# Kernel optimization log

Hardware: AMD Instinct MI355X
Metric: run time of the kernel (lower is better)

Reference implementation:

```python
import jax, jax.numpy as jnp
from jax import lax
import numpy as np

ALPHA = 0.5   # weight of shape vs temporal component
GAMMA = 0.01  # soft-min temperature
BIG = 1e10    # finite stand-in for +inf borders (safe gradients)


def _softmin3(a, b, c, gamma):
    # -gamma * logsumexp(-x/gamma) over the three candidates
    z = jnp.stack([a, b, c], axis=0)
    return -gamma * jax.nn.logsumexp(-z / gamma, axis=0)


def _softdtw(D, gamma):
    """Soft-DTW value per problem. D: (B, N, N) cost matrix -> (B,).
    Classic DP: R[i,j] = D[i-1,j-1] + softmin(R[i-1,j-1], R[i-1,j], R[i,j-1])."""
    B, N, _ = D.shape
    # R row 0: R[0,0]=0, R[0,j>=1]=inf
    row0 = jnp.concatenate(
        [jnp.zeros((B, 1), D.dtype), jnp.full((B, N), BIG, D.dtype)], axis=1)
    left_init = jnp.full((B,), BIG, D.dtype)  # R[i,0] = inf for i>=1

    def row_step(R_prev, d_row):  # d_row: (B, N) = D[:, i-1, :]
        # per column j: diag = R_prev[j-1], up = R_prev[j], left = carry
        xs = (d_row.T, R_prev[:, :-1].T, R_prev[:, 1:].T)  # each (N, B)

        def col_step(r_left, x):
            d, r_diag, r_up = x
            r = d + _softmin3(r_diag, r_up, r_left, gamma)
            return r, r

        _, vals = lax.scan(col_step, left_init, xs)  # (N, B)
        R_row = jnp.concatenate([left_init[:, None], vals.T], axis=1)  # (B, N+1)
        return R_row, None

    R_last, _ = lax.scan(row_step, row0, jnp.transpose(D, (1, 0, 2)))
    return R_last[:, -1]  # R[N, N]


def _dilate(inp, tgt):
    B, C, N = inp.shape
    t = tgt.reshape(B * C, N)
    p = inp.reshape(B * C, N)
    # pairwise squared distances between 1-d points: D[k,i,j] = (t_i - p_j)^2
    D = (t[:, :, None] - p[:, None, :]) ** 2  # (B*C, N, N)

    # shape loss = soft-DTW value, averaged over channels
    sdtw = _softdtw(D, GAMMA)  # (B*C,)
    loss_shape = sdtw.reshape(B, C).mean(axis=1)  # (B,)

    # soft alignment path = gradient of soft-DTW w.r.t. the cost matrix
    E = jax.grad(lambda d: _softdtw(d, GAMMA).sum())(D)  # (B*C, N, N)

    # Omega[i,j] = (i - j)^2 temporal penalty
    idx = jnp.arange(1, N + 1, dtype=D.dtype)
    Omega = (idx[:, None] - idx[None, :]) ** 2  # (N, N)

    lt = jnp.sum(E * Omega, axis=(1, 2)) / (N * N)  # (B*C,)
    loss_temporal = lt.reshape(B, C).mean(axis=1)  # (B,)

    loss = (ALPHA * loss_shape + (1.0 - ALPHA) * loss_temporal).mean()
    return loss, loss_shape, loss_temporal


def setup_inputs() -> dict:
    key = jax.random.key(0)
    k1, k2 = jax.random.split(key)
    B, C, N = 64, 8, 160
    return {
        "input": jax.random.normal(k1, (B, C, N), jnp.float32),
        "target": jax.random.normal(k2, (B, C, N), jnp.float32),
    }


def reference(input, target):
    return _dilate(input, target)
```

## Files before the change

kernel.cpp:

```cpp
#include <hip/hip_runtime.h>
#include <math.h>


#define NN     160
#define BC_TOT 512
#define B_SZ   64
#define C_SZ   8
#define BIGC2  1e12f
#define SC2    12.01122405f
#define GLN2   0.0069314718056f
#define KPH    16
#define NCHUNK 20
#define NPHASE 22
#define RSZ    328

__device__ __forceinline__ float fexp2(float x) {
#if __has_builtin(__builtin_amdgcn_exp2f)
    return __builtin_amdgcn_exp2f(x);
#else
    return exp2f(x);
#endif
}
__device__ __forceinline__ float flog2(float x) {
#if __has_builtin(__builtin_amdgcn_logf)
    return __builtin_amdgcn_logf(x);
#else
    return log2f(x);
#endif
}
__device__ __forceinline__ float frcp(float x) {
#if __has_builtin(__builtin_amdgcn_rcpf)
    return __builtin_amdgcn_rcpf(x);
#else
    return 1.0f / x;
#endif
}
__device__ __forceinline__ float dpp_up1_inj(float old, float x) {
    int oi = __builtin_bit_cast(int, old);
    int xi = __builtin_bit_cast(int, x);
    return __builtin_bit_cast(float,
        __builtin_amdgcn_update_dpp(oi, xi, 0x138, 0xF, 0xF, false));
}
__device__ __forceinline__ void barrier_lds() {
    __asm__ __volatile__("" ::: "memory");
    __builtin_amdgcn_s_waitcnt(0xC07F);
    __builtin_amdgcn_s_barrier();
    __asm__ __volatile__("" ::: "memory");
}

__global__ __launch_bounds__(192)
void dtw_fwd_kernel(const float* __restrict__ input,
                    const float* __restrict__ target,
                    float* __restrict__ sdtw,
                    float* __restrict__ wlt)
{
    const int k    = blockIdx.x;
    const int tid  = threadIdx.x;
    const int w    = tid >> 6;
    const int lane = tid & 63;
    const bool rowok = (tid < NN);

    __shared__ __align__(16) float  Pp[4][520];
    __shared__ __align__(16) float2 bRG[2][RSZ];

    const float* tg = target + (size_t)k * NN;
    const float* pg = input  + (size_t)k * NN;
    for (int x = tid; x < 520; x += 192) {
        #pragma unroll
        for (int s = 0; s < 4; ++s) {
            const int v = x + s - 192;
            Pp[s][x] = ((unsigned)v < (unsigned)NN) ? pg[v] * SC2 : 0.0f;
        }
    }
    for (int x = tid; x < 2 * RSZ; x += 192) {
        float2 z; z.x = BIGC2; z.y = 0.0f;
        ((float2*)bRG)[x] = z;
    }
    const float trS = rowok ? tg[tid] * SC2 : 0.0f;
    barrier_lds();

    const bool isL0    = (lane == 0);
    const bool isL63p  = (lane == 63) && (w < 2);
    const bool useRing = (w > 0);
    const int  ti2     = 2 * (tid + 1);

    const int cLoF = 4 * w;
    const int cHiF = (4 * w + 13 < NCHUNK - 1) ? 4 * w + 13 : NCHUNK - 1;

    float r1c2 = BIGC2, u1c2 = BIGC2, u2c2 = BIGC2;
    float s1 = 0.0f, v1 = 0.0f, v2 = 0.0f;

    for (int t = 0; t < NPHASE; ++t) {
        const int c = t - w;
        if (c >= cLoF && c <= cHiF) {
            const int dlo = 2 + c * KPH;
            float rgx[18], rgd[18];
            if (useRing) {
                const float4* q = (const float4*)&bRG[w - 1][dlo - 2];
                #pragma unroll
                for (int x = 0; x < 9; ++x) {
                    const float4 v4 = q[x];
                    rgx[2 * x]     = v4.x; rgd[2 * x]     = v4.y;
                    rgx[2 * x + 1] = v4.z; rgd[2 * x + 1] = v4.w;
                }
            } else {
                #pragma unroll
                for (int x = 0; x < 18; ++x) { rgx[x] = BIGC2; rgd[x] = 0.0f; }
                if (c == 0) rgx[0] = 0.0f;
            }
            float pvvS[KPH];
            {
                const int A  = 192 - tid + KPH * c;
                const int sA = A & 3;
                const float4* pq = (const float4*)&Pp[sA][A - sA];
                #pragma unroll
                for (int x = 0; x < 4; ++x) {
                    const float4 p4 = pq[x];
                    pvvS[4 * x]     = p4.x; pvvS[4 * x + 1] = p4.y;
                    pvvS[4 * x + 2] = p4.z; pvvS[4 * x + 3] = p4.w;
                }
            }
            if (c == cLoF) {
                u1c2 = isL0 ? rgx[1] : BIGC2;
                u2c2 = isL0 ? rgx[0] : BIGC2;
                v1   = isL0 ? rgd[1] : 0.0f;
                v2   = isL0 ? rgd[0] : 0.0f;
            }
            float djf = (float)(dlo - ti2);
            #pragma unroll
            for (int u = 0; u < KPH; ++u) {
                const int d = dlo + u;
                const float vdC = u2c2;
                const float vuC = u1c2;
                const float vlC = r1c2;
                const float gd = v2, gu = v1, gl = s1;
                const float mnC = fminf(vdC, fminf(vuC, vlC));
                const float ed = fexp2(mnC - vdC);
                const float ev = fexp2(mnC - vuC);
                const float eh = fexp2(mnC - vlC);
                const float ss = ed + ev + eh;
                const float rs = frcp(ss);
                const float dtS = trS - pvvS[u];
                const float rC2 = __builtin_fmaf(dtS, dtS, mnC) - flog2(ss);
                const float num = __builtin_fmaf(ed, gd,
                                  __builtin_fmaf(ev, gu, eh * gl));
                const float rdot = __builtin_fmaf(num, rs, djf * djf);
                if (isL63p) {
                    float2 pub; pub.x = rC2; pub.y = rdot;
                    bRG[w][d] = pub;
                }
                if (d == 2 * NN) {
                    if (tid == NN - 1) {
                        sdtw[k] = rC2 * GLN2;
                        wlt[k]  = rdot * (1.0f / (NN * NN));
                    }
                }
                u2c2 = u1c2;
                u1c2 = dpp_up1_inj(rgx[u + 2], rC2);
                v2 = v1;
                v1 = dpp_up1_inj(rgd[u + 2], rdot);
                r1c2 = rC2;
                s1   = rdot;
                djf += 1.0f;
            }
        }
        barrier_lds();
    }
}

__global__ __launch_bounds__(64)
void finalize_kernel(const float* __restrict__ sdtw,
                     const float* __restrict__ wlt,
                     float* __restrict__ out)
{
    const int b = threadIdx.x;
    float ls = 0.0f, lt = 0.0f;
    #pragma unroll
    for (int c = 0; c < C_SZ; ++c) {
        ls += sdtw[b * C_SZ + c];
        lt += wlt[b * C_SZ + c];
    }
    ls *= (1.0f / C_SZ);
    lt *= (1.0f / C_SZ);
    out[1 + b]        = ls;
    out[1 + B_SZ + b] = lt;
    float v = 0.5f * ls + 0.5f * lt;
    #pragma unroll
    for (int o = 32; o > 0; o >>= 1) v += __shfl_down(v, o);
    if (b == 0) out[0] = v * (1.0f / B_SZ);
}

extern "C" void kernel_launch(void* const* d_in, const int* in_sizes, int n_in,
                              void* d_out, int out_size, void* d_ws, size_t ws_size,
                              hipStream_t stream) {
    const float* input  = (const float*)d_in[0];
    const float* target = (const float*)d_in[1];
    float* out = (float*)d_out;

    float* sdtw = (float*)d_ws;
    float* wlt  = sdtw + BC_TOT;

    dtw_fwd_kernel<<<BC_TOT, 192, 0, stream>>>(input, target, sdtw, wlt);
    finalize_kernel<<<1, 64, 0, stream>>>(sdtw, wlt, out);
}
```

Baseline: 93.69 us.

## Process two DTW problems per block to interleave independent recurrences

Each block now computes two independent soft-DTW problems at once, interleaving their wavefront recurrences in the same instruction stream and halving the grid to 256 blocks. The idea is instruction-level parallelism: the serial dependency chain of exp/log/rcp per cell can be hidden by the second problem's independent work, and the per-phase barrier and ring-exchange overhead is amortised over two problems. The cost is doubled register pressure (two sets of ring and pvv arrays), wider LDS traffic, and fewer blocks, leaving 256 workgroups on a GPU with 256 CUs.

```diff
diff --git a/kernel.cpp b/kernel.cpp
--- a/kernel.cpp
+++ b/kernel.cpp
@@ -54,29 +54,34 @@
                     float* __restrict__ sdtw,
                     float* __restrict__ wlt)
 {
-    const int k    = blockIdx.x;
+    const int kA   = 2 * blockIdx.x;
     const int tid  = threadIdx.x;
     const int w    = tid >> 6;
     const int lane = tid & 63;
     const bool rowok = (tid < NN);
 
-    __shared__ __align__(16) float  Pp[4][520];
-    __shared__ __align__(16) float2 bRG[2][RSZ];
-
-    const float* tg = target + (size_t)k * NN;
-    const float* pg = input  + (size_t)k * NN;
+    __shared__ __align__(16) float  Pp[2][4][520];
+    __shared__ __align__(16) float4 bRG[2][RSZ];
+
+    const float* tgA = target + (size_t)kA * NN;
+    const float* pgA = input  + (size_t)kA * NN;
+    const float* tgB = tgA + NN;
+    const float* pgB = pgA + NN;
     for (int x = tid; x < 520; x += 192) {
         #pragma unroll
         for (int s = 0; s < 4; ++s) {
             const int v = x + s - 192;
-            Pp[s][x] = ((unsigned)v < (unsigned)NN) ? pg[v] * SC2 : 0.0f;
+            const bool ok = ((unsigned)v < (unsigned)NN);
+            Pp[0][s][x] = ok ? pgA[v] * SC2 : 0.0f;
+            Pp[1][s][x] = ok ? pgB[v] * SC2 : 0.0f;
         }
     }
     for (int x = tid; x < 2 * RSZ; x += 192) {
-        float2 z; z.x = BIGC2; z.y = 0.0f;
-        ((float2*)bRG)[x] = z;
-    }
-    const float trS = rowok ? tg[tid] * SC2 : 0.0f;
+        float4 z; z.x = BIGC2; z.y = 0.0f; z.z = BIGC2; z.w = 0.0f;
+        ((float4*)bRG)[x] = z;
+    }
+    const float trA = rowok ? tgA[tid] * SC2 : 0.0f;
+    const float trB = rowok ? tgB[tid] * SC2 : 0.0f;
     barrier_lds();
 
     const bool isL0    = (lane == 0);
@@ -87,80 +92,101 @@
     const int cLoF = 4 * w;
     const int cHiF = (4 * w + 13 < NCHUNK - 1) ? 4 * w + 13 : NCHUNK - 1;
 
-    float r1c2 = BIGC2, u1c2 = BIGC2, u2c2 = BIGC2;
-    float s1 = 0.0f, v1 = 0.0f, v2 = 0.0f;
+    float r1A = BIGC2, u1A = BIGC2, u2A = BIGC2;
+    float s1A = 0.0f,  v1A = 0.0f,  v2A = 0.0f;
+    float r1B = BIGC2, u1B = BIGC2, u2B = BIGC2;
+    float s1B = 0.0f,  v1B = 0.0f,  v2B = 0.0f;
 
     for (int t = 0; t < NPHASE; ++t) {
         const int c = t - w;
         if (c >= cLoF && c <= cHiF) {
             const int dlo = 2 + c * KPH;
-            float rgx[18], rgd[18];
+            float rgxA[18], rgdA[18], rgxB[18], rgdB[18];
             if (useRing) {
-                const float4* q = (const float4*)&bRG[w - 1][dlo - 2];
+                const float4* q = &bRG[w - 1][dlo - 2];
                 #pragma unroll
-                for (int x = 0; x < 9; ++x) {
+                for (int x = 0; x < 18; ++x) {
                     const float4 v4 = q[x];
-                    rgx[2 * x]     = v4.x; rgd[2 * x]     = v4.y;
-                    rgx[2 * x + 1] = v4.z; rgd[2 * x + 1] = v4.w;
+                    rgxA[x] = v4.x; rgdA[x] = v4.y;
+                    rgxB[x] = v4.z; rgdB[x] = v4.w;
                 }
             } else {
                 #pragma unroll
-                for (int x = 0; x < 18; ++x) { rgx[x] = BIGC2; rgd[x] = 0.0f; }
-                if (c == 0) rgx[0] = 0.0f;
-            }
-            float pvvS[KPH];
+                for (int x = 0; x < 18; ++x) {
+                    rgxA[x] = BIGC2; rgdA[x] = 0.0f;
+                    rgxB[x] = BIGC2; rgdB[x] = 0.0f;
+                }
+                if (c == 0) { rgxA[0] = 0.0f; rgxB[0] = 0.0f; }
+            }
+            float pvvA[KPH], pvvB[KPH];
             {
                 const int A  = 192 - tid + KPH * c;
                 const int sA = A & 3;
-                const float4* pq = (const float4*)&Pp[sA][A - sA];
+                const float4* qa = (const float4*)&Pp[0][sA][A - sA];
+                const float4* qb = (const float4*)&Pp[1][sA][A - sA];
                 #pragma unroll
                 for (int x = 0; x < 4; ++x) {
-                    const float4 p4 = pq[x];
-                    pvvS[4 * x]     = p4.x; pvvS[4 * x + 1] = p4.y;
-                    pvvS[4 * x + 2] = p4.z; pvvS[4 * x + 3] = p4.w;
+                    const float4 a4 = qa[x];
+                    const float4 b4 = qb[x];
+                    pvvA[4 * x]     = a4.x; pvvA[4 * x + 1] = a4.y;
+                    pvvA[4 * x + 2] = a4.z; pvvA[4 * x + 3] = a4.w;
+                    pvvB[4 * x]     = b4.x; pvvB[4 * x + 1] = b4.y;
+                    pvvB[4 * x + 2] = b4.z; pvvB[4 * x + 3] = b4.w;
                 }
             }
             if (c == cLoF) {
-                u1c2 = isL0 ? rgx[1] : BIGC2;
-                u2c2 = isL0 ? rgx[0] : BIGC2;
-                v1   = isL0 ? rgd[1] : 0.0f;
-                v2   = isL0 ? rgd[0] : 0.0f;
+                u1A = isL0 ? rgxA[1] : BIGC2;  u2A = isL0 ? rgxA[0] : BIGC2;
+                v1A = isL0 ? rgdA[1] : 0.0f;   v2A = isL0 ? rgdA[0] : 0.0f;
+                u1B = isL0 ? rgxB[1] : BIGC2;  u2B = isL0 ? rgxB[0] : BIGC2;
+                v1B = isL0 ? rgdB[1] : 0.0f;   v2B = isL0 ? rgdB[0] : 0.0f;
             }
             float djf = (float)(dlo - ti2);
             #pragma unroll
             for (int u = 0; u < KPH; ++u) {
                 const int d = dlo + u;
-                const float vdC = u2c2;
-                const float vuC = u1c2;
-                const float vlC = r1c2;
-                const float gd = v2, gu = v1, gl = s1;
-                const float mnC = fminf(vdC, fminf(vuC, vlC));
-                const float ed = fexp2(mnC - vdC);
-                const float ev = fexp2(mnC - vuC);
-                const float eh = fexp2(mnC - vlC);
-                const float ss = ed + ev + eh;
-                const float rs = frcp(ss);
-                const float dtS = trS - pvvS[u];
-                const float rC2 = __builtin_fmaf(dtS, dtS, mnC) - flog2(ss);
-                const float num = __builtin_fmaf(ed, gd,
-                                  __builtin_fmaf(ev, gu, eh * gl));
-                const float rdot = __builtin_fmaf(num, rs, djf * djf);
+                const float om = djf * djf;
+                const float mnA = fminf(u2A, fminf(u1A, r1A));
+                const float edA = fexp2(mnA - u2A);
+                const float evA = fexp2(mnA - u1A);
+                const float ehA = fexp2(mnA - r1A);
+                const float ssA = edA + evA + ehA;
+                const float rsA = frcp(ssA);
+                const float dtA = trA - pvvA[u];
+                const float rCA = __builtin_fmaf(dtA, dtA, mnA) - flog2(ssA);
+                const float numA = __builtin_fmaf(edA, v2A,
+                                   __builtin_fmaf(evA, v1A, ehA * s1A));
+                const float rdA = __builtin_fmaf(numA, rsA, om);
+                const float mnB = fminf(u2B, fminf(u1B, r1B));
+                const float edB = fexp2(mnB - u2B);
+                const float evB = fexp2(mnB - u1B);
+                const float ehB = fexp2(mnB - r1B);
+                const float ssB = edB + evB + ehB;
+                const float rsB = frcp(ssB);
+                const float dtB = trB - pvvB[u];
+                const float rCB = __builtin_fmaf(dtB, dtB, mnB) - flog2(ssB);
+                const float numB = __builtin_fmaf(edB, v2B,
+                                   __builtin_fmaf(evB, v1B, ehB * s1B));
+                const float rdB = __builtin_fmaf(numB, rsB, om);
+
                 if (isL63p) {
-                    float2 pub; pub.x = rC2; pub.y = rdot;
+                    float4 pub;
+                    pub.x = rCA; pub.y = rdA; pub.z = rCB; pub.w = rdB;
                     bRG[w][d] = pub;
                 }
                 if (d == 2 * NN) {
                     if (tid == NN - 1) {
-                        sdtw[k] = rC2 * GLN2;
-                        wlt[k]  = rdot * (1.0f / (NN * NN));
+                        sdtw[kA]     = rCA * GLN2;
+                        wlt[kA]      = rdA * (1.0f / (NN * NN));
+                        sdtw[kA + 1] = rCB * GLN2;
+                        wlt[kA + 1]  = rdB * (1.0f / (NN * NN));
                     }
                 }
-                u2c2 = u1c2;
-                u1c2 = dpp_up1_inj(rgx[u + 2], rC2);
-                v2 = v1;
-                v1 = dpp_up1_inj(rgd[u + 2], rdot);
-                r1c2 = rC2;
-                s1   = rdot;
+                u2A = u1A; u1A = dpp_up1_inj(rgxA[u + 2], rCA);
+                v2A = v1A; v1A = dpp_up1_inj(rgdA[u + 2], rdA);
+                r1A = rCA; s1A = rdA;
+                u2B = u1B; u1B = dpp_up1_inj(rgxB[u + 2], rCB);
+                v2B = v1B; v1B = dpp_up1_inj(rgdB[u + 2], rdB);
+                r1B = rCB; s1B = rdB;
                 djf += 1.0f;
             }
         }
@@ -200,6 +226,6 @@
     float* sdtw = (float*)d_ws;
     float* wlt  = sdtw + BC_TOT;
 
-    dtw_fwd_kernel<<<BC_TOT, 192, 0, stream>>>(input, target, sdtw, wlt);
+    dtw_fwd_kernel<<<BC_TOT / 2, 192, 0, stream>>>(input, target, sdtw, wlt);
     finalize_kernel<<<1, 64, 0, stream>>>(sdtw, wlt, out);
 }
```

After: 105.6 us. 12.7% more time.

## Process all row bands in one wavefront sequentially, dropping inter-wave barriers

Applied to the files above, without the earlier changes.

Each block now runs a single 64-lane wavefront that works through the three 64-row bands one after another, instead of three wavefronts pipelined across phases with a block barrier after every phase. The boundary ring buffer shrinks to one shared row, overwritten in place. The next chunk's LDS window is double-buffered into registers before the current chunk is computed. This removes barrier and idle-wave cost but makes each block's serial dependency chain longer, since the bands no longer overlap in time.

```diff
diff --git a/kernel.cpp b/kernel.cpp
--- a/kernel.cpp
+++ b/kernel.cpp
@@ -10,8 +10,6 @@
 #define SC2    12.01122405f
 #define GLN2   0.0069314718056f
 #define KPH    16
-#define NCHUNK 20
-#define NPHASE 22
 #define RSZ    328
 
 __device__ __forceinline__ float fexp2(float x) {
@@ -48,123 +46,120 @@
     __asm__ __volatile__("" ::: "memory");
 }
 
-__global__ __launch_bounds__(192)
+#define LOAD_WIN(c_, rgx_, rgd_, pvv_) do {                                   \
+    const int dlo_ = 2 + (c_) * KPH;                                          \
+    if (w > 0) {                                                              \
+        const float4* q_ = (const float4*)&bRG[dlo_ - 2];                     \
+        _Pragma("unroll")                                                     \
+        for (int x_ = 0; x_ < 9; ++x_) {                                      \
+            const float4 v4_ = q_[x_];                                        \
+            rgx_[2 * x_]     = v4_.x; rgd_[2 * x_]     = v4_.y;               \
+            rgx_[2 * x_ + 1] = v4_.z; rgd_[2 * x_ + 1] = v4_.w;               \
+        }                                                                     \
+    } else {                                                                  \
+        _Pragma("unroll")                                                     \
+        for (int x_ = 0; x_ < 18; ++x_) { rgx_[x_] = BIGC2; rgd_[x_] = 0.0f; }\
+        if ((c_) == 0) rgx_[0] = 0.0f;           \
+    }                                                                         \
+    const int A_  = 192 - (64 * w + lane) + KPH * (c_);                       \
+    const int sA_ = A_ & 3;                                                   \
+    const float4* pq_ = (const float4*)&Pp[sA_][A_ - sA_];                    \
+    _Pragma("unroll")                                                         \
+    for (int x_ = 0; x_ < 4; ++x_) {                                          \
+        const float4 p4_ = pq_[x_];                                           \
+        pvv_[4 * x_]     = p4_.x; pvv_[4 * x_ + 1] = p4_.y;                   \
+        pvv_[4 * x_ + 2] = p4_.z; pvv_[4 * x_ + 3] = p4_.w;                   \
+    }                                                                         \
+} while (0)
+
+#define COMP_CHUNK(c_, rgx_, rgd_, pvv_) do {                                 \
+    const int dlo_ = 2 + (c_) * KPH;                                          \
+    if ((c_) == cLo) {         \
+        u1 = isL0 ? rgx_[1] : BIGC2;  u2 = isL0 ? rgx_[0] : BIGC2;            \
+        v1 = isL0 ? rgd_[1] : 0.0f;   v2 = isL0 ? rgd_[0] : 0.0f;             \
+    }                                                                         \
+    float djf_ = (float)(dlo_ - ti2);                       \
+    _Pragma("unroll")                                                         \
+    for (int u_ = 0; u_ < KPH; ++u_) {                                        \
+        const int d_ = dlo_ + u_;                                             \
+        const float mn = fminf(u2, fminf(u1, r1));                            \
+        const float ed = fexp2(mn - u2);         \
+        const float ev = fexp2(mn - u1);                                      \
+        const float eh = fexp2(mn - r1);                                      \
+        const float ss = ed + ev + eh;                              \
+        const float rs = frcp(ss);                                            \
+        const float dt = trS - pvv_[u_];                                      \
+        const float rC = __builtin_fmaf(dt, dt, mn) - flog2(ss);              \
+        const float nm = __builtin_fmaf(ed, v2,                               \
+                         __builtin_fmaf(ev, v1, eh * s1));                    \
+        const float rd = __builtin_fmaf(nm, rs, djf_ * djf_);                 \
+        if (pub) { float2 pb; pb.x = rC; pb.y = rd; bRG[d_] = pb; }           \
+        if (d_ == 2 * NN) {                                                   \
+            if (w == 2 && lane == NN - 1 - 128) {         \
+                sdtw[k] = rC * GLN2;                                          \
+                wlt[k]  = rd * (1.0f / (NN * NN));                            \
+            }                                                                 \
+        }                                                                     \
+        u2 = u1; u1 = dpp_up1_inj(rgx_[u_ + 2], rC);     \
+        v2 = v1; v1 = dpp_up1_inj(rgd_[u_ + 2], rd);                          \
+        r1 = rC; s1 = rd;                                                     \
+        djf_ += 1.0f;                                                         \
+    }                                                                         \
+} while (0)
+
+__global__ __launch_bounds__(64)
 void dtw_fwd_kernel(const float* __restrict__ input,
                     const float* __restrict__ target,
                     float* __restrict__ sdtw,
                     float* __restrict__ wlt)
 {
     const int k    = blockIdx.x;
-    const int tid  = threadIdx.x;
-    const int w    = tid >> 6;
-    const int lane = tid & 63;
-    const bool rowok = (tid < NN);
+    const int lane = threadIdx.x;
 
     __shared__ __align__(16) float  Pp[4][520];
-    __shared__ __align__(16) float2 bRG[2][RSZ];
+    __shared__ __align__(16) float2 bRG[RSZ];
 
     const float* tg = target + (size_t)k * NN;
     const float* pg = input  + (size_t)k * NN;
-    for (int x = tid; x < 520; x += 192) {
+    for (int x = lane; x < 520; x += 64) {
         #pragma unroll
         for (int s = 0; s < 4; ++s) {
             const int v = x + s - 192;
             Pp[s][x] = ((unsigned)v < (unsigned)NN) ? pg[v] * SC2 : 0.0f;
         }
     }
-    for (int x = tid; x < 2 * RSZ; x += 192) {
+    for (int x = lane; x < RSZ; x += 64) {
         float2 z; z.x = BIGC2; z.y = 0.0f;
-        ((float2*)bRG)[x] = z;
-    }
-    const float trS = rowok ? tg[tid] * SC2 : 0.0f;
+        bRG[x] = z;
+    }
+    const float tr0 = tg[lane] * SC2;
+    const float tr1 = tg[64 + lane] * SC2;
+    const float tr2 = (lane < NN - 128) ? tg[128 + lane] * SC2 : 0.0f;
     barrier_lds();
 
-    const bool isL0    = (lane == 0);
-    const bool isL63p  = (lane == 63) && (w < 2);
-    const bool useRing = (w > 0);
-    const int  ti2     = 2 * (tid + 1);
-
-    const int cLoF = 4 * w;
-    const int cHiF = (4 * w + 13 < NCHUNK - 1) ? 4 * w + 13 : NCHUNK - 1;
-
-    float r1c2 = BIGC2, u1c2 = BIGC2, u2c2 = BIGC2;
-    float s1 = 0.0f, v1 = 0.0f, v2 = 0.0f;
-
-    for (int t = 0; t < NPHASE; ++t) {
-        const int c = t - w;
-        if (c >= cLoF && c <= cHiF) {
-            const int dlo = 2 + c * KPH;
-            float rgx[18], rgd[18];
-            if (useRing) {
-                const float4* q = (const float4*)&bRG[w - 1][dlo - 2];
-                #pragma unroll
-                for (int x = 0; x < 9; ++x) {
-                    const float4 v4 = q[x];
-                    rgx[2 * x]     = v4.x; rgd[2 * x]     = v4.y;
-                    rgx[2 * x + 1] = v4.z; rgd[2 * x + 1] = v4.w;
-                }
-            } else {
-                #pragma unroll
-                for (int x = 0; x < 18; ++x) { rgx[x] = BIGC2; rgd[x] = 0.0f; }
-                if (c == 0) rgx[0] = 0.0f;
-            }
-            float pvvS[KPH];
-            {
-                const int A  = 192 - tid + KPH * c;
-                const int sA = A & 3;
-                const float4* pq = (const float4*)&Pp[sA][A - sA];
-                #pragma unroll
-                for (int x = 0; x < 4; ++x) {
-                    const float4 p4 = pq[x];
-                    pvvS[4 * x]     = p4.x; pvvS[4 * x + 1] = p4.y;
-                    pvvS[4 * x + 2] = p4.z; pvvS[4 * x + 3] = p4.w;
-                }
-            }
-            if (c == cLoF) {
-                u1c2 = isL0 ? rgx[1] : BIGC2;
-                u2c2 = isL0 ? rgx[0] : BIGC2;
-                v1   = isL0 ? rgd[1] : 0.0f;
-                v2   = isL0 ? rgd[0] : 0.0f;
-            }
-            float djf = (float)(dlo - ti2);
-            #pragma unroll
-            for (int u = 0; u < KPH; ++u) {
-                const int d = dlo + u;
-                const float vdC = u2c2;
-                const float vuC = u1c2;
-                const float vlC = r1c2;
-                const float gd = v2, gu = v1, gl = s1;
-                const float mnC = fminf(vdC, fminf(vuC, vlC));
-                const float ed = fexp2(mnC - vdC);
-                const float ev = fexp2(mnC - vuC);
-                const float eh = fexp2(mnC - vlC);
-                const float ss = ed + ev + eh;
-                const float rs = frcp(ss);
-                const float dtS = trS - pvvS[u];
-                const float rC2 = __builtin_fmaf(dtS, dtS, mnC) - flog2(ss);
-                const float num = __builtin_fmaf(ed, gd,
-                                  __builtin_fmaf(ev, gu, eh * gl));
-                const float rdot = __builtin_fmaf(num, rs, djf * djf);
-                if (isL63p) {
-                    float2 pub; pub.x = rC2; pub.y = rdot;
-                    bRG[w][d] = pub;
-                }
-                if (d == 2 * NN) {
-                    if (tid == NN - 1) {
-                        sdtw[k] = rC2 * GLN2;
-                        wlt[k]  = rdot * (1.0f / (NN * NN));
-                    }
-                }
-                u2c2 = u1c2;
-                u1c2 = dpp_up1_inj(rgx[u + 2], rC2);
-                v2 = v1;
-                v1 = dpp_up1_inj(rgd[u + 2], rdot);
-                r1c2 = rC2;
-                s1   = rdot;
-                djf += 1.0f;
-            }
+    const bool isL0 = (lane == 0);
+
+    for (int w = 0; w < 3; ++w) {
+        __asm__ __volatile__("" ::: "memory");
+        const int  cLo = 4 * w;
+        const int  cHi = (4 * w + 13 < 19) ? 4 * w + 13 : 19;
+        const bool pub = (lane == 63) && (w < 2);
+        const float trS = (w == 0) ? tr0 : (w == 1) ? tr1 : tr2;
+        const int  ti2 = 2 * (64 * w + lane + 1);
+
+        float r1 = BIGC2, u1 = BIGC2, u2 = BIGC2;
+        float s1 = 0.0f,  v1 = 0.0f,  v2 = 0.0f;
+
+        float rgxA[18], rgdA[18], pvvA[16];
+        float rgxB[18], rgdB[18], pvvB[16];
+
+        LOAD_WIN(cLo, rgxA, rgdA, pvvA);
+        for (int c = cLo; c <= cHi; c += 2) {
+            LOAD_WIN(c + 1, rgxB, rgdB, pvvB);
+            COMP_CHUNK(c, rgxA, rgdA, pvvA);
+            if (c + 2 <= cHi) LOAD_WIN(c + 2, rgxA, rgdA, pvvA);
+            COMP_CHUNK(c + 1, rgxB, rgdB, pvvB);
         }
-        barrier_lds();
     }
 }
 
@@ -200,6 +195,6 @@
     float* sdtw = (float*)d_ws;
     float* wlt  = sdtw + BC_TOT;
 
-    dtw_fwd_kernel<<<BC_TOT, 192, 0, stream>>>(input, target, sdtw, wlt);
+    dtw_fwd_kernel<<<BC_TOT, 64, 0, stream>>>(input, target, sdtw, wlt);
     finalize_kernel<<<1, 64, 0, stream>>>(sdtw, wlt, out);
 }
```

After: 110.7 us. +18.1%, slower.

## Replace block barriers with LDS flag spin-waits between wavefronts in soft-DTW wavefront

Applied to the files above, without the earlier changes.

Block-wide barriers per phase are replaced by per-wave progress flags in LDS. Each downstream wave spins on its upstream wave's counter before reading the boundary ring. The chunk size is halved to 8 anti-diagonals, so the pipeline fill skew between the three waves shrinks. The ring buffer is no longer initialized, and correctness relies on ordering of the publishing lane's LDS writes before the flag store. Spin-polling adds LDS traffic and the risk of subtle visibility issues.

```diff
diff --git a/kernel.cpp b/kernel.cpp
--- a/kernel.cpp
+++ b/kernel.cpp
@@ -9,10 +9,9 @@
 #define BIGC2  1e12f
 #define SC2    12.01122405f
 #define GLN2   0.0069314718056f
-#define KPH    16
-#define NCHUNK 20
-#define NPHASE 22
-#define RSZ    328
+#define KPH    8
+#define NCH    28
+#define RSZ    360
 
 __device__ __forceinline__ float fexp2(float x) {
 #if __has_builtin(__builtin_amdgcn_exp2f)
@@ -48,7 +47,7 @@
     __asm__ __volatile__("" ::: "memory");
 }
 
-__global__ __launch_bounds__(192)
+__global__ __launch_bounds__(192, 1)
 void dtw_fwd_kernel(const float* __restrict__ input,
                     const float* __restrict__ target,
                     float* __restrict__ sdtw,
@@ -58,10 +57,10 @@
     const int tid  = threadIdx.x;
     const int w    = tid >> 6;
     const int lane = tid & 63;
-    const bool rowok = (tid < NN);
 
     __shared__ __align__(16) float  Pp[4][520];
     __shared__ __align__(16) float2 bRG[2][RSZ];
+    __shared__ int flags[2];
 
     const float* tg = target + (size_t)k * NN;
     const float* pg = input  + (size_t)k * NN;
@@ -72,99 +71,105 @@
             Pp[s][x] = ((unsigned)v < (unsigned)NN) ? pg[v] * SC2 : 0.0f;
         }
     }
-    for (int x = tid; x < 2 * RSZ; x += 192) {
-        float2 z; z.x = BIGC2; z.y = 0.0f;
-        ((float2*)bRG)[x] = z;
-    }
-    const float trS = rowok ? tg[tid] * SC2 : 0.0f;
+    if (tid < 2) flags[tid] = 0;
+    const float trS = (tid < NN) ? tg[tid] * SC2 : 0.0f;
     barrier_lds();
 
     const bool isL0    = (lane == 0);
-    const bool isL63p  = (lane == 63) && (w < 2);
-    const bool useRing = (w > 0);
+    const bool pubw    = (w < 2);
+    const bool isL63p  = (lane == 63) && pubw;
     const int  ti2     = 2 * (tid + 1);
-
-    const int cLoF = 4 * w;
-    const int cHiF = (4 * w + 13 < NCHUNK - 1) ? 4 * w + 13 : NCHUNK - 1;
-
-    float r1c2 = BIGC2, u1c2 = BIGC2, u2c2 = BIGC2;
-    float s1 = 0.0f, v1 = 0.0f, v2 = 0.0f;
-
-    for (int t = 0; t < NPHASE; ++t) {
-        const int c = t - w;
-        if (c >= cLoF && c <= cHiF) {
-            const int dlo = 2 + c * KPH;
-            float rgx[18], rgd[18];
-            if (useRing) {
-                const float4* q = (const float4*)&bRG[w - 1][dlo - 2];
-                #pragma unroll
-                for (int x = 0; x < 9; ++x) {
-                    const float4 v4 = q[x];
-                    rgx[2 * x]     = v4.x; rgd[2 * x]     = v4.y;
-                    rgx[2 * x + 1] = v4.z; rgd[2 * x + 1] = v4.w;
+    const int  c0      = 8 * w;
+    const unsigned fPrevA = (unsigned)(unsigned long long)&flags[(w > 0) ? (w - 1) : 0];
+
+    float r1 = BIGC2, u1 = BIGC2, u2 = BIGC2;
+    float s1 = 0.0f,  v1 = 0.0f,  v2 = 0.0f;
+
+    for (int c = c0; c < c0 + NCH; ++c) {
+        if (w > 0) {
+            int fv;
+            for (;;) {
+                asm volatile("ds_read_b32 %0, %1\n\ts_waitcnt lgkmcnt(0)"
+                             : "=v"(fv) : "v"(fPrevA) : "memory");
+                if (__builtin_amdgcn_readfirstlane(fv) >= c + 1) break;
+            }
+        }
+        const int dlo = 2 + c * KPH;
+        float rgx[10], rgd[10];
+        if (w > 0) {
+            const float4* q = (const float4*)&bRG[w - 1][dlo - 2];
+            #pragma unroll
+            for (int x = 0; x < 5; ++x) {
+                const float4 v4 = q[x];
+                rgx[2 * x]     = v4.x; rgd[2 * x]     = v4.y;
+                rgx[2 * x + 1] = v4.z; rgd[2 * x + 1] = v4.w;
+            }
+        } else {
+            #pragma unroll
+            for (int x = 0; x < 10; ++x) { rgx[x] = BIGC2; rgd[x] = 0.0f; }
+            if (c == 0) rgx[0] = 0.0f;
+        }
+        float pvv[KPH];
+        {
+            const int A  = 192 - tid + KPH * c;
+            const int sA = A & 3;
+            const float4* pq = (const float4*)&Pp[sA][A - sA];
+            #pragma unroll
+            for (int x = 0; x < 2; ++x) {
+                const float4 p4 = pq[x];
+                pvv[4 * x]     = p4.x; pvv[4 * x + 1] = p4.y;
+                pvv[4 * x + 2] = p4.z; pvv[4 * x + 3] = p4.w;
+            }
+        }
+        if (c == c0) {
+            u1 = isL0 ? rgx[1] : BIGC2;  u2 = isL0 ? rgx[0] : BIGC2;
+            v1 = isL0 ? rgd[1] : 0.0f;   v2 = isL0 ? rgd[0] : 0.0f;
+        }
+        float djf = (float)(dlo - ti2);
+        #pragma unroll
+        for (int u = 0; u < KPH; ++u) {
+            const int d = dlo + u;
+            const float vdC = u2;
+            const float vuC = u1;
+            const float vlC = r1;
+            const float gd = v2, gu = v1, gl = s1;
+            const float mnC = fminf(vdC, fminf(vuC, vlC));
+            const float ed = fexp2(mnC - vdC);
+            const float ev = fexp2(mnC - vuC);
+            const float eh = fexp2(mnC - vlC);
+            const float ss = ed + ev + eh;
+            const float rs = frcp(ss);
+            const float dtS = trS - pvv[u];
+            const float rC2 = __builtin_fmaf(dtS, dtS, mnC) - flog2(ss);
+            const float num = __builtin_fmaf(ed, gd,
+                              __builtin_fmaf(ev, gu, eh * gl));
+            const float rdot = __builtin_fmaf(num, rs, djf * djf);
+            if (isL63p) {
+                float2 pb; pb.x = rC2; pb.y = rdot;
+                bRG[w][d] = pb;
+            }
+            if (d == 2 * NN) {
+                if (tid == NN - 1) {
+                    sdtw[k] = rC2 * GLN2;
+                    wlt[k]  = rdot * (1.0f / (NN * NN));
                 }
-            } else {
-                #pragma unroll
-                for (int x = 0; x < 18; ++x) { rgx[x] = BIGC2; rgd[x] = 0.0f; }
-                if (c == 0) rgx[0] = 0.0f;
-            }
-            float pvvS[KPH];
-            {
-                const int A  = 192 - tid + KPH * c;
-                const int sA = A & 3;
-                const float4* pq = (const float4*)&Pp[sA][A - sA];
-                #pragma unroll
-                for (int x = 0; x < 4; ++x) {
-                    const float4 p4 = pq[x];
-                    pvvS[4 * x]     = p4.x; pvvS[4 * x + 1] = p4.y;
-                    pvvS[4 * x + 2] = p4.z; pvvS[4 * x + 3] = p4.w;
-                }
-            }
-            if (c == cLoF) {
-                u1c2 = isL0 ? rgx[1] : BIGC2;
-                u2c2 = isL0 ? rgx[0] : BIGC2;
-                v1   = isL0 ? rgd[1] : 0.0f;
-                v2   = isL0 ? rgd[0] : 0.0f;
-            }
-            float djf = (float)(dlo - ti2);
-            #pragma unroll
-            for (int u = 0; u < KPH; ++u) {
-                const int d = dlo + u;
-                const float vdC = u2c2;
-                const float vuC = u1c2;
-                const float vlC = r1c2;
-                const float gd = v2, gu = v1, gl = s1;
-                const float mnC = fminf(vdC, fminf(vuC, vlC));
-                const float ed = fexp2(mnC - vdC);
-                const float ev = fexp2(mnC - vuC);
-                const float eh = fexp2(mnC - vlC);
-                const float ss = ed + ev + eh;
-                const float rs = frcp(ss);
-                const float dtS = trS - pvvS[u];
-                const float rC2 = __builtin_fmaf(dtS, dtS, mnC) - flog2(ss);
-                const float num = __builtin_fmaf(ed, gd,
-                                  __builtin_fmaf(ev, gu, eh * gl));
-                const float rdot = __builtin_fmaf(num, rs, djf * djf);
-                if (isL63p) {
-                    float2 pub; pub.x = rC2; pub.y = rdot;
-                    bRG[w][d] = pub;
-                }
-                if (d == 2 * NN) {
-                    if (tid == NN - 1) {
-                        sdtw[k] = rC2 * GLN2;
-                        wlt[k]  = rdot * (1.0f / (NN * NN));
-                    }
-                }
-                u2c2 = u1c2;
-                u1c2 = dpp_up1_inj(rgx[u + 2], rC2);
-                v2 = v1;
-                v1 = dpp_up1_inj(rgd[u + 2], rdot);
-                r1c2 = rC2;
-                s1   = rdot;
-                djf += 1.0f;
-            }
-        }
-        barrier_lds();
+            }
+            u2 = u1;
+            u1 = dpp_up1_inj(rgx[u + 2], rC2);
+            v2 = v1;
+            v1 = dpp_up1_inj(rgd[u + 2], rdot);
+            r1 = rC2;
+            s1 = rdot;
+            djf += 1.0f;
+        }
+        if (pubw) {
+            asm volatile("s_waitcnt lgkmcnt(0)" ::: "memory");
+            if (lane == 0) *(volatile int*)&flags[w] = c + 1;
+        }
+    }
+    if (pubw) {
+        asm volatile("s_waitcnt lgkmcnt(0)" ::: "memory");
+        if (lane == 0) *(volatile int*)&flags[w] = 1 << 20;
     }
 }
 
```

Measured after the change: 102.7 us. 9.6% more time.
